# Kernel optimization log

Hardware: AMD Instinct MI355X
Metric: run time of the kernel (lower is better)

Reference implementation:

```python
import jax, jax.numpy as jnp
import numpy as np

N_STATE = 64   # S4 state size N
L_MAX = 4096   # sequence length
H = 256        # number of SSM channels (d_model)
BATCH = 16


def _green_roots(Lambda, P, B, C, step, L):
    """Frequency-domain S4 kernel at the L roots of unity (Q = P, DPLR).
    Lambda,P,B,C: complex[N]; step: scalar. Returns complex[L]."""
    Omega = jnp.exp(-2j * jnp.pi * (jnp.arange(L) / L))          # (L,)
    g = (2.0 / step) * ((1.0 - Omega) / (1.0 + Omega))           # (L,)
    c = 2.0 / (1.0 + Omega)                                      # (L,)
    # four Cauchy numerators stacked: k00,k01,k10,k11
    vs = jnp.stack([C.conj() * B, C.conj() * P,
                    P.conj() * B, P.conj() * P])                 # (4,N)
    denom = g[:, None] - Lambda[None, :]                         # (L,N)
    k = jnp.einsum('kn,ln->kl', vs, 1.0 / denom)                 # (4,L)
    k00, k01, k10, k11 = k
    return c * (k00 - k01 * (1.0 / (1.0 + k11)) * k10)           # (L,)


def _kernel_freq(Lambda_re, Lambda_im, P_re, P_im, B_re, B_im,
                 C_re, C_im, log_step, L):
    Lambda = (Lambda_re + 1j * Lambda_im).astype(jnp.complex64)  # (H,N)
    P = (P_re + 1j * P_im).astype(jnp.complex64)
    Bm = (B_re + 1j * B_im).astype(jnp.complex64)
    Cm = (C_re + 1j * C_im).astype(jnp.complex64)
    step = jnp.exp(log_step)                                     # (H,)
    f = lambda lam, p, b, c, s: _green_roots(lam, p, b, c, s, L)
    return jax.vmap(f)(Lambda, P, Bm, Cm, step)                  # (H,L)


def setup_inputs() -> dict:
    key = jax.random.key(0)
    ks = jax.random.split(key, 10)
    u = jax.random.normal(ks[0], (BATCH, H, L_MAX), dtype=jnp.float32)
    # stable continuous-time poles: negative real part, spread imag parts
    Lambda_re = -0.5 * jnp.ones((H, N_STATE), jnp.float32) \
        - jax.random.uniform(ks[1], (H, N_STATE), dtype=jnp.float32)
    Lambda_im = jnp.pi * jax.random.normal(ks[2], (H, N_STATE), dtype=jnp.float32) * N_STATE / 8
    scale = 1.0 / np.sqrt(N_STATE)
    P_re = scale * jax.random.normal(ks[3], (H, N_STATE), dtype=jnp.float32)
    P_im = scale * jax.random.normal(ks[4], (H, N_STATE), dtype=jnp.float32)
    B_re = scale * jax.random.normal(ks[5], (H, N_STATE), dtype=jnp.float32)
    B_im = scale * jax.random.normal(ks[6], (H, N_STATE), dtype=jnp.float32)
    C_re = scale * jax.random.normal(ks[7], (H, N_STATE), dtype=jnp.float32)
    C_im = scale * jax.random.normal(ks[8], (H, N_STATE), dtype=jnp.float32)
    # log-uniform step in [1e-3, 1e-1] (log_step_initializer)
    log_step = (jax.random.uniform(ks[9], (H,), dtype=jnp.float32)
                * (np.log(0.1) - np.log(0.001)) + np.log(0.001)).astype(jnp.float32)
    return {"u": u, "Lambda_re": Lambda_re, "Lambda_im": Lambda_im,
            "P_re": P_re, "P_im": P_im, "B_re": B_re, "B_im": B_im,
            "C_re": C_re, "C_im": C_im, "log_step": log_step}


def reference(u, Lambda_re, Lambda_im, P_re, P_im, B_re, B_im,
              C_re, C_im, log_step):
    L = u.shape[-1]
    Kf = _kernel_freq(Lambda_re, Lambda_im, P_re, P_im, B_re, B_im,
                      C_re, C_im, log_step, L)                   # (H,L) complex
    # circular_convolution_complex, batched over (BATCH,H)
    ud = jnp.fft.fft(u, axis=-1)                                  # (B,H,L)
    y = jnp.fft.ifft(ud * Kf[None, :, :], n=L, axis=-1)
    return y.real.astype(jnp.float32)                             # (B,H,L)
```

## Files before the change

kernel.cpp:

```cpp
#include <hip/hip_runtime.h>
#include <math.h>

#define NSTATE 64
#define LEN    4096
#define NH     256
#define NB     16

__device__ float2 g_knat[NH * LEN];
__device__ float2 g_ksym[NH * LEN];
__device__ float4 g_pA[NH * NSTATE];
__device__ float4 g_pB[NH * NSTATE];
__device__ float2 g_pC[NH * NSTATE];

__device__ __forceinline__ int rev8_12(int p) {
  return ((p & 7) << 9) | (((p >> 3) & 7) << 6) | (((p >> 6) & 7) << 3) | (p >> 9);
}

__device__ __forceinline__ float2 cadd(float2 a, float2 b){ return make_float2(a.x+b.x, a.y+b.y); }
__device__ __forceinline__ float2 csub(float2 a, float2 b){ return make_float2(a.x-b.x, a.y-b.y); }
__device__ __forceinline__ float2 cmul(float2 a, float2 b){ return make_float2(a.x*b.x - a.y*b.y, a.x*b.y + a.y*b.x); }
__device__ __forceinline__ float2 mulnegi(float2 a){ return make_float2(a.y, -a.x); }
__device__ __forceinline__ float2 mulposi(float2 a){ return make_float2(-a.y, a.x); }

#define RSQ2 0.70710678118654752f

__device__ __forceinline__ void bfly8_fwd(float2 v[8]) {
  float2 a0 = cadd(v[0], v[4]), b0 = csub(v[0], v[4]);
  float2 a1 = cadd(v[1], v[5]), d1 = csub(v[1], v[5]);
  float2 a2 = cadd(v[2], v[6]), d2 = csub(v[2], v[6]);
  float2 a3 = cadd(v[3], v[7]), d3 = csub(v[3], v[7]);
  float2 b1 = make_float2(RSQ2 * (d1.x + d1.y), RSQ2 * (d1.y - d1.x));
  float2 b2 = mulnegi(d2);
  float2 b3 = make_float2(RSQ2 * (d3.y - d3.x), -RSQ2 * (d3.x + d3.y));
  float2 u0 = cadd(a0, a2), u1 = csub(a0, a2), u2 = cadd(a1, a3), u3 = csub(a1, a3);
  v[0] = cadd(u0, u2);
  v[2] = cadd(u1, mulnegi(u3));
  v[4] = csub(u0, u2);
  v[6] = cadd(u1, mulposi(u3));
  float2 w0 = cadd(b0, b2), w1 = csub(b0, b2), w2 = cadd(b1, b3), w3 = csub(b1, b3);
  v[1] = cadd(w0, w2);
  v[3] = cadd(w1, mulnegi(w3));
  v[5] = csub(w0, w2);
  v[7] = cadd(w1, mulposi(w3));
}

__device__ __forceinline__ void bfly8_inv(float2 v[8]) {
  float2 a0 = cadd(v[0], v[4]), b0 = csub(v[0], v[4]);
  float2 a1 = cadd(v[1], v[5]), d1 = csub(v[1], v[5]);
  float2 a2 = cadd(v[2], v[6]), d2 = csub(v[2], v[6]);
  float2 a3 = cadd(v[3], v[7]), d3 = csub(v[3], v[7]);
  float2 b1 = make_float2(RSQ2 * (d1.x - d1.y), RSQ2 * (d1.x + d1.y));
  float2 b2 = mulposi(d2);
  float2 b3 = make_float2(-RSQ2 * (d3.x + d3.y), RSQ2 * (d3.x - d3.y));
  float2 u0 = cadd(a0, a2), u1 = csub(a0, a2), u2 = cadd(a1, a3), u3 = csub(a1, a3);
  v[0] = cadd(u0, u2);
  v[2] = cadd(u1, mulposi(u3));
  v[4] = csub(u0, u2);
  v[6] = cadd(u1, mulnegi(u3));
  float2 w0 = cadd(b0, b2), w1 = csub(b0, b2), w2 = cadd(b1, b3), w3 = csub(b1, b3);
  v[1] = cadd(w0, w2);
  v[3] = cadd(w1, mulposi(w3));
  v[5] = csub(w0, w2);
  v[7] = cadd(w1, mulnegi(w3));
}

__device__ __forceinline__ void twiddle7(float2 v[8], float wr, float wi) {
  float2 w1 = make_float2(wr, wi);
  float2 w2 = cmul(w1, w1);
  float2 w3 = cmul(w2, w1);
  float2 w4 = cmul(w2, w2);
  float2 w5 = cmul(w3, w2);
  float2 w6 = cmul(w3, w3);
  float2 w7 = cmul(w4, w3);
  v[1] = cmul(v[1], w1); v[2] = cmul(v[2], w2); v[3] = cmul(v[3], w3);
  v[4] = cmul(v[4], w4); v[5] = cmul(v[5], w5); v[6] = cmul(v[6], w6);
  v[7] = cmul(v[7], w7);
}

__global__ __launch_bounds__(256) void s4_prep(
    const float* __restrict__ Lre, const float* __restrict__ Lim,
    const float* __restrict__ Pre, const float* __restrict__ Pim,
    const float* __restrict__ Bre, const float* __restrict__ Bim,
    const float* __restrict__ Cre, const float* __restrict__ Cim)
{
  int idx = blockIdx.x * 256 + threadIdx.x;
  if (idx >= NH * NSTATE) return;
  float lr = Lre[idx], li = Lim[idx];
  float pr = Pre[idx], pi = Pim[idx];
  float br = Bre[idx], bi = Bim[idx];
  float cr = Cre[idx], ci = Cim[idx];
  g_pA[idx] = make_float4(lr, li, pr * pr + pi * pi, 0.0f);
  g_pB[idx] = make_float4(cr * br + ci * bi, cr * bi - ci * br,
                          cr * pr + ci * pi, cr * pi - ci * pr);
  g_pC[idx] = make_float2(pr * br + pi * bi, pr * bi - pi * br);
}

__global__ __launch_bounds__(256) void s4_kernel_freq(const float* __restrict__ log_step)
{
  const int b = blockIdx.x;
  const int h = b >> 2;
  const int q = ((b & 3) << 8) | threadIdx.x;
  const float step = expf(log_step[h]);
  const float ts = 2.0f / step;
  const float NEG2PI = -6.2831853071795864769f;

  float gar, gai, car, cai, gbr, gbi, cbr, cbi;
  float gcr, gci, ccr, cci, gdr, gdi, cdr, cdi;
  {
    float so, co;
    sincosf(NEG2PI * ((float)q * (1.0f / (float)LEN)), &so, &co);
    float dr = 1.0f + co, di = so;
    float inv = 1.0f / fmaf(dr, dr, di * di);
    car = 2.0f * dr * inv; cai = -2.0f * di * inv;
    float nr = 1.0f - co, ni = -so;
    gar = ts * (fmaf(nr, dr, ni * di) * inv);
    gai = ts * (fmaf(ni, dr, -nr * di) * inv);
  }
  if (q == 0) {
    float so, co;
    sincosf(NEG2PI * 0.5f, &so, &co);
    float dr = 1.0f + co, di = so;
    float inv = 1.0f / fmaf(dr, dr, di * di);
    cbr = 2.0f * dr * inv; cbi = -2.0f * di * inv;
    float nr = 1.0f - co, ni = -so;
    gbr = ts * (fmaf(nr, dr, ni * di) * inv);
    gbi = ts * (fmaf(ni, dr, -nr * di) * inv);
  } else {
    gbr = gar; gbi = -gai; cbr = car; cbi = -cai;
  }
  {
    float so, co;
    sincosf(NEG2PI * ((float)(q + 1024) * (1.0f / (float)LEN)), &so, &co);
    float dr = 1.0f + co, di = so;
    float inv = 1.0f / fmaf(dr, dr, di * di);
    ccr = 2.0f * dr * inv; cci = -2.0f * di * inv;
    float nr = 1.0f - co, ni = -so;
    gcr = ts * (fmaf(nr, dr, ni * di) * inv);
    gci = ts * (fmaf(ni, dr, -nr * di) * inv);
  }
  gdr = gcr; gdi = -gci; cdr = ccr; cdi = -cci;

  float A00r=0,A00i=0,A01r=0,A01i=0,A10r=0,A10i=0,A11r=0,A11i=0;
  float B00r=0,B00i=0,B01r=0,B01i=0,B10r=0,B10i=0,B11r=0,B11i=0;
  float C00r=0,C00i=0,C01r=0,C01i=0,C10r=0,C10i=0,C11r=0,C11i=0;
  float D00r=0,D00i=0,D01r=0,D01i=0,D10r=0,D10i=0,D11r=0,D11i=0;

  const float4* __restrict__ pa = g_pA + h * NSTATE;
  const float4* __restrict__ pb = g_pB + h * NSTATE;
  const float2* __restrict__ pc = g_pC + h * NSTATE;

#define CAUCHY(gre, gim, k00r,k00i,k01r,k01i,k10r,k10i,k11r,k11i)            \
  {                                                                          \
    float rd = gre - Av.x, id = gim - Av.y;                                  \
    float idn = __builtin_amdgcn_rcpf(fmaf(rd, rd, id * id));                \
    float ir = rd * idn, ii = -(id * idn);                                   \
    k00r = fmaf(Bv.x, ir, k00r); k00r = fmaf(-Bv.y, ii, k00r);               \
    k00i = fmaf(Bv.x, ii, k00i); k00i = fmaf(Bv.y, ir, k00i);                \
    k01r = fmaf(Bv.z, ir, k01r); k01r = fmaf(-Bv.w, ii, k01r);               \
    k01i = fmaf(Bv.z, ii, k01i); k01i = fmaf(Bv.w, ir, k01i);                \
    k10r = fmaf(Cv.x, ir, k10r); k10r = fmaf(-Cv.y, ii, k10r);               \
    k10i = fmaf(Cv.x, ii, k10i); k10i = fmaf(Cv.y, ir, k10i);                \
    k11r = fmaf(Av.z, ir, k11r); k11i = fmaf(Av.z, ii, k11i);                \
  }

#pragma unroll 4
  for (int n = 0; n < NSTATE; ++n) {
    float4 Av = pa[n];
    float4 Bv = pb[n];
    float2 Cv = pc[n];
    CAUCHY(gar, gai, A00r,A00i,A01r,A01i,A10r,A10i,A11r,A11i)
    CAUCHY(gbr, gbi, B00r,B00i,B01r,B01i,B10r,B10i,B11r,B11i)
    CAUCHY(gcr, gci, C00r,C00i,C01r,C01i,C10r,C10i,C11r,C11i)
    CAUCHY(gdr, gdi, D00r,D00i,D01r,D01i,D10r,D10i,D11r,D11i)
  }
#undef CAUCHY

#define FINISH(cr_, ci_, k00r,k00i,k01r,k01i,k10r,k10i,k11r,k11i, Kr, Ki)    \
  {                                                                          \
    float rr = 1.0f + k11r, ri = k11i;                                       \
    float rinv = 1.0f / fmaf(rr, rr, ri * ri);                               \
    float pr_ = k01r * k10r - k01i * k10i;                                   \
    float pi_ = k01r * k10i + k01i * k10r;                                   \
    float wr = (pr_ * rr + pi_ * ri) * rinv;                                 \
    float wi = (pi_ * rr - pr_ * ri) * rinv;                                 \
    float sr = k00r - wr, si = k00i - wi;                                    \
    Kr = cr_ * sr - ci_ * si; Ki = cr_ * si + ci_ * sr;                      \
  }

  float Kar, Kai, Kbr, Kbi, Kcr, Kci, Kdr, Kdi;
  FINISH(car, cai, A00r,A00i,A01r,A01i,A10r,A10i,A11r,A11i, Kar, Kai)
  FINISH(cbr, cbi, B00r,B00i,B01r,B01i,B10r,B10i,B11r,B11i, Kbr, Kbi)
  FINISH(ccr, cci, C00r,C00i,C01r,C01i,C10r,C10i,C11r,C11i, Kcr, Kci)
  FINISH(cdr, cdi, D00r,D00i,D01r,D01i,D10r,D10i,D11r,D11i, Kdr, Kdi)
#undef FINISH

  float2* out = g_knat + (size_t)h * LEN;
  if (q == 0) {
    out[0]    = make_float2(Kar, 0.0f);
    out[2048] = make_float2(Kbr, 0.0f);
  } else {
    float fr = 0.5f * (Kar + Kbr), fi = 0.5f * (Kai - Kbi);
    out[q]        = make_float2(fr, fi);
    out[LEN - q]  = make_float2(fr, -fi);
  }
  {
    float fr = 0.5f * (Kcr + Kdr), fi = 0.5f * (Kci - Kdi);
    out[1024 + q] = make_float2(fr, fi);
    out[3072 - q] = make_float2(fr, -fi);
  }
}

__global__ __launch_bounds__(256) void s4_reorder()
{
  __shared__ float2 s[LEN];
  const int h = blockIdx.x, t = threadIdx.x;
  const float2* __restrict__ in = g_knat + (size_t)h * LEN;
  float2* __restrict__ out = g_ksym + (size_t)h * LEN;
  for (int i = t; i < LEN; i += 256) s[i ^ ((i >> 6) & 63)] = in[i];
  __syncthreads();
  for (int p = t; p < LEN; p += 256) {
    int l = rev8_12(p);
    out[p] = s[l ^ ((l >> 6) & 63)];
  }
}

__global__ __launch_bounds__(512) void s4_fftconv(const float* __restrict__ u,
                                                 float* __restrict__ y)
{
  __shared__ float2 X[4608];

  const int t = threadIdx.x;
  const int bid = blockIdx.x;
  const int h  = bid & (NH - 1);
  const int bp = bid >> 8;

  float c1, s1, c2, s2, c3, s3;
  sincosf((float)t         * (-6.2831853071795864769f / 4096.0f), &s1, &c1);
  sincosf((float)(t & 63)  * (-6.2831853071795864769f /  512.0f), &s2, &c2);
  sincosf((float)(t & 7)   * (-6.2831853071795864769f /   64.0f), &s3, &c3);

  const float* u1 = u + ((size_t)bp * NH + h) * LEN;
  const float* u2 = u + ((size_t)(bp + 8) * NH + h) * LEN;

  float2 v[8];
#pragma unroll
  for (int m = 0; m < 8; ++m)
    v[m] = make_float2(u1[t + 512 * m], u2[t + 512 * m]);
  bfly8_fwd(v);
  twiddle7(v, c1, s1);
#pragma unroll
  for (int m = 0; m < 8; ++m) X[t + 512 * m] = v[m];
  __syncthreads();

  {
    int B = t >> 6, j = t & 63, base = B * 512 + j;
#pragma unroll
    for (int m = 0; m < 8; ++m) v[m] = X[base + 64 * m];
  }
  __syncthreads();
  bfly8_fwd(v);
  twiddle7(v, c2, s2);
  {
    int B = t >> 6, j = t & 63;
#pragma unroll
    for (int m = 0; m < 8; ++m) X[68 * (8 * B + m) + j] = v[m];
  }
  __syncthreads();

  {
    int b = t >> 3, j = t & 7;
#pragma unroll
    for (int m = 0; m < 8; ++m) v[m] = X[68 * b + j + 8 * m];
  }
  __syncthreads();
  bfly8_fwd(v);
  twiddle7(v, c3, s3);
  {
    int b = t >> 3, j = t & 7;
#pragma unroll
    for (int m = 0; m < 8; ++m) X[9 * (8 * b + m) + j] = v[m];
  }
  __syncthreads();

  {
    const float4* kp = (const float4*)(g_ksym + (size_t)h * LEN + 8 * t);
    float4 k0 = kp[0], k1 = kp[1], k2 = kp[2], k3 = kp[3];
#pragma unroll
    for (int m = 0; m < 8; ++m) v[m] = X[9 * t + m];
    bfly8_fwd(v);
    v[0] = cmul(v[0], make_float2(k0.x, k0.y));
    v[1] = cmul(v[1], make_float2(k0.z, k0.w));
    v[2] = cmul(v[2], make_float2(k1.x, k1.y));
    v[3] = cmul(v[3], make_float2(k1.z, k1.w));
    v[4] = cmul(v[4], make_float2(k2.x, k2.y));
    v[5] = cmul(v[5], make_float2(k2.z, k2.w));
    v[6] = cmul(v[6], make_float2(k3.x, k3.y));
    v[7] = cmul(v[7], make_float2(k3.z, k3.w));
    bfly8_inv(v);
#pragma unroll
    for (int p = 0; p < 8; ++p) X[9 * t + p] = v[p];
  }
  __syncthreads();

  {
    int b = t >> 3, j = t & 7;
#pragma unroll
    for (int m = 0; m < 8; ++m) v[m] = X[9 * (8 * b + m) + j];
  }
  twiddle7(v, c3, -s3);
  bfly8_inv(v);
  __syncthreads();
  {
    int b = t >> 3, j = t & 7;
#pragma unroll
    for (int p = 0; p < 8; ++p) X[68 * b + j + 8 * p] = v[p];
  }
  __syncthreads();

  {
    int B = t >> 6, j = t & 63;
#pragma unroll
    for (int m = 0; m < 8; ++m) v[m] = X[68 * (8 * B + m) + j];
  }
  twiddle7(v, c2, -s2);
  bfly8_inv(v);
  __syncthreads();
  {
    int B = t >> 6, j = t & 63, base = B * 512 + j;
#pragma unroll
    for (int p = 0; p < 8; ++p) X[base + 64 * p] = v[p];
  }
  __syncthreads();

#pragma unroll
  for (int m = 0; m < 8; ++m) v[m] = X[t + 512 * m];
  twiddle7(v, c1, -s1);
  bfly8_inv(v);

  float* y1 = y + ((size_t)bp * NH + h) * LEN;
  float* y2 = y + ((size_t)(bp + 8) * NH + h) * LEN;
  const float sc = 1.0f / (float)LEN;
#pragma unroll
  for (int p = 0; p < 8; ++p) {
    y1[t + 512 * p] = v[p].x * sc;
    y2[t + 512 * p] = v[p].y * sc;
  }
}

extern "C" void kernel_launch(void* const* d_in, const int* in_sizes, int n_in,
                              void* d_out, int out_size, void* d_ws, size_t ws_size,
                              hipStream_t stream) {
  const float* u    = (const float*)d_in[0];
  const float* Lre  = (const float*)d_in[1];
  const float* Lim  = (const float*)d_in[2];
  const float* Pre  = (const float*)d_in[3];
  const float* Pim  = (const float*)d_in[4];
  const float* Bre  = (const float*)d_in[5];
  const float* Bim  = (const float*)d_in[6];
  const float* Cre  = (const float*)d_in[7];
  const float* Cim  = (const float*)d_in[8];
  const float* lstep = (const float*)d_in[9];
  float* y = (float*)d_out;

  s4_prep<<<(NH * NSTATE + 255) / 256, 256, 0, stream>>>(Lre, Lim, Pre, Pim, Bre, Bim, Cre, Cim);
  s4_kernel_freq<<<NH * 4, 256, 0, stream>>>(lstep);
  s4_reorder<<<NH, 256, 0, stream>>>();
  s4_fftconv<<<NH * (NB / 2), 512, 0, stream>>>(u, y);
}
```

Before: 184.6 us.

## Switch FFT convolution from radix-8 four-pass to radix-16 three-pass with 256 threads

Replaces the 4096-point radix-8 FFT (four passes, 512 threads, padded shared memory) with a radix-16 decomposition in three passes using 256 threads. Shared-memory bank conflicts are now avoided with an XOR swizzle instead of padding. The 1/L scale is folded into the kernel spectrum in the reorder kernel rather than applied per output. The goal is fewer shared-memory round trips and barriers, and less shared memory per block. In exchange each thread holds more registers (16 complex values plus 8 float4), and launch bounds of 256 threads with 5 blocks per CU are requested.

```diff
diff --git a/kernel.cpp b/kernel.cpp
--- a/kernel.cpp
+++ b/kernel.cpp
@@ -12,10 +12,6 @@
 __device__ float4 g_pB[NH * NSTATE];
 __device__ float2 g_pC[NH * NSTATE];
 
-__device__ __forceinline__ int rev8_12(int p) {
-  return ((p & 7) << 9) | (((p >> 3) & 7) << 6) | (((p >> 6) & 7) << 3) | (p >> 9);
-}
-
 __device__ __forceinline__ float2 cadd(float2 a, float2 b){ return make_float2(a.x+b.x, a.y+b.y); }
 __device__ __forceinline__ float2 csub(float2 a, float2 b){ return make_float2(a.x-b.x, a.y-b.y); }
 __device__ __forceinline__ float2 cmul(float2 a, float2 b){ return make_float2(a.x*b.x - a.y*b.y, a.x*b.y + a.y*b.x); }
@@ -23,58 +19,81 @@
 __device__ __forceinline__ float2 mulposi(float2 a){ return make_float2(-a.y, a.x); }
 
 #define RSQ2 0.70710678118654752f
-
-__device__ __forceinline__ void bfly8_fwd(float2 v[8]) {
-  float2 a0 = cadd(v[0], v[4]), b0 = csub(v[0], v[4]);
-  float2 a1 = cadd(v[1], v[5]), d1 = csub(v[1], v[5]);
-  float2 a2 = cadd(v[2], v[6]), d2 = csub(v[2], v[6]);
-  float2 a3 = cadd(v[3], v[7]), d3 = csub(v[3], v[7]);
-  float2 b1 = make_float2(RSQ2 * (d1.x + d1.y), RSQ2 * (d1.y - d1.x));
-  float2 b2 = mulnegi(d2);
-  float2 b3 = make_float2(RSQ2 * (d3.y - d3.x), -RSQ2 * (d3.x + d3.y));
-  float2 u0 = cadd(a0, a2), u1 = csub(a0, a2), u2 = cadd(a1, a3), u3 = csub(a1, a3);
-  v[0] = cadd(u0, u2);
-  v[2] = cadd(u1, mulnegi(u3));
-  v[4] = csub(u0, u2);
-  v[6] = cadd(u1, mulposi(u3));
-  float2 w0 = cadd(b0, b2), w1 = csub(b0, b2), w2 = cadd(b1, b3), w3 = csub(b1, b3);
-  v[1] = cadd(w0, w2);
-  v[3] = cadd(w1, mulnegi(w3));
-  v[5] = csub(w0, w2);
-  v[7] = cadd(w1, mulposi(w3));
-}
-
-__device__ __forceinline__ void bfly8_inv(float2 v[8]) {
-  float2 a0 = cadd(v[0], v[4]), b0 = csub(v[0], v[4]);
-  float2 a1 = cadd(v[1], v[5]), d1 = csub(v[1], v[5]);
-  float2 a2 = cadd(v[2], v[6]), d2 = csub(v[2], v[6]);
-  float2 a3 = cadd(v[3], v[7]), d3 = csub(v[3], v[7]);
-  float2 b1 = make_float2(RSQ2 * (d1.x - d1.y), RSQ2 * (d1.x + d1.y));
-  float2 b2 = mulposi(d2);
-  float2 b3 = make_float2(-RSQ2 * (d3.x + d3.y), RSQ2 * (d3.x - d3.y));
-  float2 u0 = cadd(a0, a2), u1 = csub(a0, a2), u2 = cadd(a1, a3), u3 = csub(a1, a3);
-  v[0] = cadd(u0, u2);
-  v[2] = cadd(u1, mulposi(u3));
-  v[4] = csub(u0, u2);
-  v[6] = cadd(u1, mulnegi(u3));
-  float2 w0 = cadd(b0, b2), w1 = csub(b0, b2), w2 = cadd(b1, b3), w3 = csub(b1, b3);
-  v[1] = cadd(w0, w2);
-  v[3] = cadd(w1, mulposi(w3));
-  v[5] = csub(w0, w2);
-  v[7] = cadd(w1, mulnegi(w3));
-}
-
-__device__ __forceinline__ void twiddle7(float2 v[8], float wr, float wi) {
-  float2 w1 = make_float2(wr, wi);
-  float2 w2 = cmul(w1, w1);
-  float2 w3 = cmul(w2, w1);
-  float2 w4 = cmul(w2, w2);
-  float2 w5 = cmul(w3, w2);
-  float2 w6 = cmul(w3, w3);
-  float2 w7 = cmul(w4, w3);
-  v[1] = cmul(v[1], w1); v[2] = cmul(v[2], w2); v[3] = cmul(v[3], w3);
-  v[4] = cmul(v[4], w4); v[5] = cmul(v[5], w5); v[6] = cmul(v[6], w6);
-  v[7] = cmul(v[7], w7);
+#define C16  0.92387953251128675613f
+#define S16  0.38268343236508977173f
+
+__device__ __forceinline__ void bfly16_fwd(float2 v[16]) {
+#pragma unroll
+  for (int n1 = 0; n1 < 4; ++n1) {
+    float2 a=v[n1], b=v[n1+4], c=v[n1+8], d=v[n1+12];
+    float2 t0=cadd(a,c), t1=csub(a,c), t2=cadd(b,d), t3=csub(b,d);
+    v[n1]    = cadd(t0,t2);
+    v[n1+4]  = cadd(t1, mulnegi(t3));
+    v[n1+8]  = csub(t0,t2);
+    v[n1+12] = cadd(t1, mulposi(t3));
+  }
+  v[5]  = cmul(v[5],  make_float2(C16,-S16));
+  v[9]  = make_float2(RSQ2*(v[9].x + v[9].y),  RSQ2*(v[9].y - v[9].x));
+  v[13] = cmul(v[13], make_float2(S16,-C16));
+  v[6]  = make_float2(RSQ2*(v[6].x + v[6].y),  RSQ2*(v[6].y - v[6].x));
+  v[10] = mulnegi(v[10]);
+  v[14] = make_float2(RSQ2*(v[14].y - v[14].x), -RSQ2*(v[14].x + v[14].y));
+  v[7]  = cmul(v[7],  make_float2(S16,-C16));
+  v[11] = make_float2(RSQ2*(v[11].y - v[11].x), -RSQ2*(v[11].x + v[11].y));
+  v[15] = cmul(v[15], make_float2(-C16,S16));
+  float2 r[16];
+#pragma unroll
+  for (int k2 = 0; k2 < 4; ++k2) {
+    float2 a=v[4*k2], b=v[4*k2+1], c=v[4*k2+2], d=v[4*k2+3];
+    float2 t0=cadd(a,c), t1=csub(a,c), t2=cadd(b,d), t3=csub(b,d);
+    r[k2]    = cadd(t0,t2);
+    r[k2+4]  = cadd(t1, mulnegi(t3));
+    r[k2+8]  = csub(t0,t2);
+    r[k2+12] = cadd(t1, mulposi(t3));
+  }
+#pragma unroll
+  for (int i = 0; i < 16; ++i) v[i] = r[i];
+}
+
+__device__ __forceinline__ void bfly16_inv(float2 v[16]) {
+#pragma unroll
+  for (int n1 = 0; n1 < 4; ++n1) {
+    float2 a=v[n1], b=v[n1+4], c=v[n1+8], d=v[n1+12];
+    float2 t0=cadd(a,c), t1=csub(a,c), t2=cadd(b,d), t3=csub(b,d);
+    v[n1]    = cadd(t0,t2);
+    v[n1+4]  = cadd(t1, mulposi(t3));
+    v[n1+8]  = csub(t0,t2);
+    v[n1+12] = cadd(t1, mulnegi(t3));
+  }
+  v[5]  = cmul(v[5],  make_float2(C16,S16));
+  v[9]  = make_float2(RSQ2*(v[9].x - v[9].y),  RSQ2*(v[9].x + v[9].y));
+  v[13] = cmul(v[13], make_float2(S16,C16));
+  v[6]  = make_float2(RSQ2*(v[6].x - v[6].y),  RSQ2*(v[6].x + v[6].y));
+  v[10] = mulposi(v[10]);
+  v[14] = make_float2(-RSQ2*(v[14].x + v[14].y), RSQ2*(v[14].x - v[14].y));
+  v[7]  = cmul(v[7],  make_float2(S16,C16));
+  v[11] = make_float2(-RSQ2*(v[11].x + v[11].y), RSQ2*(v[11].x - v[11].y));
+  v[15] = cmul(v[15], make_float2(-C16,-S16));
+  float2 r[16];
+#pragma unroll
+  for (int k2 = 0; k2 < 4; ++k2) {
+    float2 a=v[4*k2], b=v[4*k2+1], c=v[4*k2+2], d=v[4*k2+3];
+    float2 t0=cadd(a,c), t1=csub(a,c), t2=cadd(b,d), t3=csub(b,d);
+    r[k2]    = cadd(t0,t2);
+    r[k2+4]  = cadd(t1, mulposi(t3));
+    r[k2+8]  = csub(t0,t2);
+    r[k2+12] = cadd(t1, mulnegi(t3));
+  }
+#pragma unroll
+  for (int i = 0; i < 16; ++i) v[i] = r[i];
+}
+
+__device__ __forceinline__ void twiddle15(float2 v[16], float wr, float wi) {
+  float2 w = make_float2(wr, wi);
+  float2 p = w;
+  v[1] = cmul(v[1], p);
+#pragma unroll
+  for (int m = 2; m < 16; ++m) { p = cmul(p, w); v[m] = cmul(v[m], p); }
 }
 
 __global__ __launch_bounds__(256) void s4_prep(
@@ -216,134 +235,92 @@
   const int h = blockIdx.x, t = threadIdx.x;
   const float2* __restrict__ in = g_knat + (size_t)h * LEN;
   float2* __restrict__ out = g_ksym + (size_t)h * LEN;
-  for (int i = t; i < LEN; i += 256) s[i ^ ((i >> 6) & 63)] = in[i];
-  __syncthreads();
+  for (int i = t; i < LEN; i += 256) s[i ^ ((i >> 8) & 15)] = in[i];
+  __syncthreads();
+  const float sc = 1.0f / (float)LEN;
   for (int p = t; p < LEN; p += 256) {
-    int l = rev8_12(p);
-    out[p] = s[l ^ ((l >> 6) & 63)];
-  }
-}
-
-__global__ __launch_bounds__(512) void s4_fftconv(const float* __restrict__ u,
-                                                 float* __restrict__ y)
+    int f = ((p & 15) << 8) | (p & 0xF0) | (p >> 8);
+    float2 k = s[f ^ ((f >> 8) & 15)];
+    out[p] = make_float2(k.x * sc, k.y * sc);
+  }
+}
+
+#define PH(a) ((a) ^ (((a) >> 4) & 15))
+
+__global__ __launch_bounds__(256, 5) void s4_fftconv(const float* __restrict__ u,
+                                                    float* __restrict__ y)
 {
-  __shared__ float2 X[4608];
+  __shared__ float2 X[LEN];
 
   const int t = threadIdx.x;
   const int bid = blockIdx.x;
   const int h  = bid & (NH - 1);
   const int bp = bid >> 8;
 
-  float c1, s1, c2, s2, c3, s3;
-  sincosf((float)t         * (-6.2831853071795864769f / 4096.0f), &s1, &c1);
-  sincosf((float)(t & 63)  * (-6.2831853071795864769f /  512.0f), &s2, &c2);
-  sincosf((float)(t & 7)   * (-6.2831853071795864769f /   64.0f), &s3, &c3);
+  float cA, sA, cB, sB;
+  sincosf((float)t        * (-6.2831853071795864769f / 4096.0f), &sA, &cA);
+  sincosf((float)(t & 15) * (-6.2831853071795864769f /  256.0f), &sB, &cB);
 
   const float* u1 = u + ((size_t)bp * NH + h) * LEN;
   const float* u2 = u + ((size_t)(bp + 8) * NH + h) * LEN;
 
-  float2 v[8];
-#pragma unroll
-  for (int m = 0; m < 8; ++m)
-    v[m] = make_float2(u1[t + 512 * m], u2[t + 512 * m]);
-  bfly8_fwd(v);
-  twiddle7(v, c1, s1);
-#pragma unroll
-  for (int m = 0; m < 8; ++m) X[t + 512 * m] = v[m];
+  float2 v[16];
+#pragma unroll
+  for (int m = 0; m < 16; ++m)
+    v[m] = make_float2(u1[t + 256 * m], u2[t + 256 * m]);
+  bfly16_fwd(v);
+  twiddle15(v, cA, sA);
+#pragma unroll
+  for (int m = 0; m < 16; ++m) { int a = t + 256 * m; X[PH(a)] = v[m]; }
+  __syncthreads();
+
+  const int baseB = (t >> 4) * 256 + (t & 15);
+#pragma unroll
+  for (int s = 0; s < 16; ++s) { int a = baseB + 16 * s; v[s] = X[PH(a)]; }
+  bfly16_fwd(v);
+  twiddle15(v, cB, sB);
+#pragma unroll
+  for (int n = 0; n < 16; ++n) { int a = baseB + 16 * n; X[PH(a)] = v[n]; }
   __syncthreads();
 
   {
-    int B = t >> 6, j = t & 63, base = B * 512 + j;
-#pragma unroll
-    for (int m = 0; m < 8; ++m) v[m] = X[base + 64 * m];
-  }
-  __syncthreads();
-  bfly8_fwd(v);
-  twiddle7(v, c2, s2);
-  {
-    int B = t >> 6, j = t & 63;
-#pragma unroll
-    for (int m = 0; m < 8; ++m) X[68 * (8 * B + m) + j] = v[m];
-  }
-  __syncthreads();
-
-  {
-    int b = t >> 3, j = t & 7;
-#pragma unroll
-    for (int m = 0; m < 8; ++m) v[m] = X[68 * b + j + 8 * m];
-  }
-  __syncthreads();
-  bfly8_fwd(v);
-  twiddle7(v, c3, s3);
-  {
-    int b = t >> 3, j = t & 7;
-#pragma unroll
-    for (int m = 0; m < 8; ++m) X[9 * (8 * b + m) + j] = v[m];
-  }
-  __syncthreads();
-
-  {
-    const float4* kp = (const float4*)(g_ksym + (size_t)h * LEN + 8 * t);
-    float4 k0 = kp[0], k1 = kp[1], k2 = kp[2], k3 = kp[3];
-#pragma unroll
-    for (int m = 0; m < 8; ++m) v[m] = X[9 * t + m];
-    bfly8_fwd(v);
-    v[0] = cmul(v[0], make_float2(k0.x, k0.y));
-    v[1] = cmul(v[1], make_float2(k0.z, k0.w));
-    v[2] = cmul(v[2], make_float2(k1.x, k1.y));
-    v[3] = cmul(v[3], make_float2(k1.z, k1.w));
-    v[4] = cmul(v[4], make_float2(k2.x, k2.y));
-    v[5] = cmul(v[5], make_float2(k2.z, k2.w));
-    v[6] = cmul(v[6], make_float2(k3.x, k3.y));
-    v[7] = cmul(v[7], make_float2(k3.z, k3.w));
-    bfly8_inv(v);
-#pragma unroll
-    for (int p = 0; p < 8; ++p) X[9 * t + p] = v[p];
-  }
-  __syncthreads();
-
-  {
-    int b = t >> 3, j = t & 7;
-#pragma unroll
-    for (int m = 0; m < 8; ++m) v[m] = X[9 * (8 * b + m) + j];
-  }
-  twiddle7(v, c3, -s3);
-  bfly8_inv(v);
-  __syncthreads();
-  {
-    int b = t >> 3, j = t & 7;
-#pragma unroll
-    for (int p = 0; p < 8; ++p) X[68 * b + j + 8 * p] = v[p];
-  }
-  __syncthreads();
-
-  {
-    int B = t >> 6, j = t & 63;
-#pragma unroll
-    for (int m = 0; m < 8; ++m) v[m] = X[68 * (8 * B + m) + j];
-  }
-  twiddle7(v, c2, -s2);
-  bfly8_inv(v);
-  __syncthreads();
-  {
-    int B = t >> 6, j = t & 63, base = B * 512 + j;
-#pragma unroll
-    for (int p = 0; p < 8; ++p) X[base + 64 * p] = v[p];
-  }
-  __syncthreads();
-
-#pragma unroll
-  for (int m = 0; m < 8; ++m) v[m] = X[t + 512 * m];
-  twiddle7(v, c1, -s1);
-  bfly8_inv(v);
+    const float4* kp = (const float4*)(g_ksym + (size_t)h * LEN + 16 * t);
+    float4 kq[8];
+#pragma unroll
+    for (int i = 0; i < 8; ++i) kq[i] = kp[i];
+#pragma unroll
+    for (int k = 0; k < 16; ++k) { int a = 16 * t + k; v[k] = X[PH(a)]; }
+    bfly16_fwd(v);
+#pragma unroll
+    for (int i = 0; i < 8; ++i) {
+      v[2*i]   = cmul(v[2*i],   make_float2(kq[i].x, kq[i].y));
+      v[2*i+1] = cmul(v[2*i+1], make_float2(kq[i].z, kq[i].w));
+    }
+    bfly16_inv(v);
+#pragma unroll
+    for (int k = 0; k < 16; ++k) { int a = 16 * t + k; X[PH(a)] = v[k]; }
+  }
+  __syncthreads();
+
+#pragma unroll
+  for (int n = 0; n < 16; ++n) { int a = baseB + 16 * n; v[n] = X[PH(a)]; }
+  twiddle15(v, cB, -sB);
+  bfly16_inv(v);
+#pragma unroll
+  for (int s = 0; s < 16; ++s) { int a = baseB + 16 * s; X[PH(a)] = v[s]; }
+  __syncthreads();
+
+#pragma unroll
+  for (int m = 0; m < 16; ++m) { int a = t + 256 * m; v[m] = X[PH(a)]; }
+  twiddle15(v, cA, -sA);
+  bfly16_inv(v);
 
   float* y1 = y + ((size_t)bp * NH + h) * LEN;
   float* y2 = y + ((size_t)(bp + 8) * NH + h) * LEN;
-  const float sc = 1.0f / (float)LEN;
-#pragma unroll
-  for (int p = 0; p < 8; ++p) {
-    y1[t + 512 * p] = v[p].x * sc;
-    y2[t + 512 * p] = v[p].y * sc;
+#pragma unroll
+  for (int s = 0; s < 16; ++s) {
+    y1[t + 256 * s] = v[s].x;
+    y2[t + 256 * s] = v[s].y;
   }
 }
 
@@ -365,5 +342,5 @@
   s4_prep<<<(NH * NSTATE + 255) / 256, 256, 0, stream>>>(Lre, Lim, Pre, Pim, Bre, Bim, Cre, Cim);
   s4_kernel_freq<<<NH * 4, 256, 0, stream>>>(lstep);
   s4_reorder<<<NH, 256, 0, stream>>>();
-  s4_fftconv<<<NH * (NB / 2), 512, 0, stream>>>(u, y);
-}
+  s4_fftconv<<<NH * (NB / 2), 256, 0, stream>>>(u, y);
+}
```

Result: slower. 248.4 us (+34.6%).
